# Performance work log

Measured on AMD Instinct MI355X. Metric: run time of the kernel, lower is better.

Reference implementation:

```python
import jax, jax.numpy as jnp
import numpy as np

# dims (match init_kwargs / input_specs)
B, T = 32, 512
DIM, DEPTH, HEADS, NB_FEAT, N_MASKS = 256, 6, 8, 128, 4
DIM_HEAD = DIM // HEADS  # 32
FF_MULT = 4
KERNEL_EPS = 1e-4


def _orth_proj(key, m, d):
    # FAVOR+ gaussian orthogonal random features: stacked QR blocks, row norms from fresh gaussians
    nb = m // d
    keys = jax.random.split(key, nb + 1)
    blocks = []
    for i in range(nb):
        g = jax.random.normal(keys[i], (d, d))
        q, _ = jnp.linalg.qr(g)
        blocks.append(q.T)
    proj = jnp.concatenate(blocks, axis=0)  # (m, d)
    norms = jnp.linalg.norm(jax.random.normal(keys[-1], (m, d)), axis=-1)
    return (proj * norms[:, None]).astype(jnp.float32)


def setup_inputs() -> dict:
    key = jax.random.key(0)
    ks = jax.random.split(key, 12)
    init = lambda k, sh: (jax.random.normal(k, sh, dtype=jnp.float32) * 0.02)
    L = DEPTH
    return {
        "mel": jax.random.normal(ks[0], (B, DIM, T), dtype=jnp.float32),
        "proj": _orth_proj(ks[1], NB_FEAT, DIM_HEAD),
        "ln1_g": jnp.ones((L, DIM), jnp.float32), "ln1_b": jnp.zeros((L, DIM), jnp.float32),
        "Wq": init(ks[2], (L, DIM, DIM)), "Wk": init(ks[3], (L, DIM, DIM)),
        "Wv": init(ks[4], (L, DIM, DIM)),
        "Wo": init(ks[5], (L, DIM, DIM)), "bo": jnp.zeros((L, DIM), jnp.float32),
        "ln2_g": jnp.ones((L, DIM), jnp.float32), "ln2_b": jnp.zeros((L, DIM), jnp.float32),
        "W1": init(ks[6], (L, DIM, FF_MULT * DIM)), "b1": jnp.zeros((L, FF_MULT * DIM), jnp.float32),
        "W2": init(ks[7], (L, FF_MULT * DIM, DIM)), "b2": jnp.zeros((L, DIM), jnp.float32),
        "Wm": init(ks[8], (DIM, N_MASKS)), "bm": jnp.zeros((N_MASKS,), jnp.float32),
    }


def _ln(x, g, b):
    mu = jnp.mean(x, -1, keepdims=True)
    var = jnp.var(x, -1, keepdims=True)
    return (x - mu) * jax.lax.rsqrt(var + 1e-5) * g + b


def _softmax_kernel(x, proj, is_query):
    # x: (B,H,N,dh), proj: (m,dh)
    dn = x.shape[-1] ** -0.25
    ratio = proj.shape[0] ** -0.5
    xd = jnp.einsum('bhnd,md->bhnm', x * dn, proj)
    diag = 0.5 * jnp.sum(jnp.square(x * dn), axis=-1, keepdims=True)
    if is_query:
        mx = jnp.max(xd, axis=-1, keepdims=True)
    else:
        mx = jnp.max(xd, axis=(-1, -2), keepdims=True)
    return ratio * (jnp.exp(xd - diag - mx) + KERNEL_EPS)


def _split_heads(x):
    b, n, _ = x.shape
    return x.reshape(b, n, HEADS, DIM_HEAD).transpose(0, 2, 1, 3)  # (B,H,N,dh)


def _forward(mel, proj, ln1_g, ln1_b, Wq, Wk, Wv, Wo, bo, ln2_g, ln2_b, W1, b1, W2, b2, Wm, bm):
    x = jnp.transpose(mel, (0, 2, 1))  # (B, T, DIM)
    for l in range(DEPTH):
        # --- FAVOR+ self-attention (pre-LN, non-causal linear attention) ---
        h = _ln(x, ln1_g[l], ln1_b[l])
        q = _split_heads(h @ Wq[l])
        k = _split_heads(h @ Wk[l])
        v = _split_heads(h @ Wv[l])
        qp = _softmax_kernel(q, proj, True)   # (B,H,T,m)
        kp = _softmax_kernel(k, proj, False)  # (B,H,T,m)
        ctx = jnp.einsum('bhnm,bhnd->bhmd', kp, v)          # (B,H,m,dh)
        o = jnp.einsum('bhnm,bhmd->bhnd', qp, ctx)          # (B,H,T,dh)
        denom = jnp.einsum('bhnm,bhm->bhn', qp, kp.sum(axis=2))
        o = o / denom[..., None]
        o = o.transpose(0, 2, 1, 3).reshape(x.shape[0], x.shape[1], DIM)
        x = x + o @ Wo[l] + bo[l]
        h = _ln(x, ln2_g[l], ln2_b[l])
        x = x + jax.nn.gelu(h @ W1[l] + b1[l]) @ W2[l] + b2[l]
    masks = x @ Wm + bm                  # (B, T, M)
    return jnp.transpose(masks, (0, 2, 1))  # (B, M, T)


def reference(mel, proj, ln1_g, ln1_b, Wq, Wk, Wv, Wo, bo, ln2_g, ln2_b, W1, b1, W2, b2, Wm, bm):
    return _forward(mel, proj, ln1_g, ln1_b, Wq, Wk, Wv, Wo, bo, ln2_g, ln2_b, W1, b1, W2, b2, Wm, bm)
```

## Files before the change

kernel.cpp:

```cpp
#include <hip/hip_runtime.h>
#include <math.h>

#define B 32
#define T 512
#define D 256
#define H 8
#define DH 32
#define MF 128
#define NLAYER 6
#define FF 1024
#define NM 4
#define BT (B*T)
#define BH (B*H)

#define DN2H 0.08838834764831845f
#define DNS  0.4204482076268573f
#define RATIO 0.08838834764831845f
#define KEPS 1e-4f

typedef __attribute__((ext_vector_type(8))) short short8;
typedef __attribute__((ext_vector_type(4))) float f32x4;

#define MFMA(a, b, c) __builtin_amdgcn_mfma_f32_16x16x32_bf16(a, b, c, 0, 0, 0)

#define SWZG(l) (((((l) & 3) + (((l) >> 3) & 3)) & 3) * 8)
#define RS(li, gi) (((((gi) - ((li) >> 1)) & 3)) * 8)

#define WAIT_VM(N) asm volatile("s_waitcnt vmcnt(" #N ")" ::: "memory")

__device__ __forceinline__ ushort f2b(float x) {
  union { float f; unsigned u; } c; c.f = x;
  unsigned r = (c.u + 0x7FFFu + ((c.u >> 16) & 1u)) >> 16;
  return (ushort)r;
}
__device__ __forceinline__ float bf2f(ushort u) {
  union { unsigned u; float f; } c; c.u = ((unsigned)u) << 16;
  return c.f;
}
__device__ __forceinline__ void gload16(const ushort* g, ushort* l) {
  __builtin_amdgcn_global_load_lds((const __attribute__((address_space(1))) void*)g,
                                   (__attribute__((address_space(3))) void*)l, 16, 0, 0);
}

__global__ void transpose_mel(const float* __restrict__ mel, float* __restrict__ x) {
  __shared__ float tile[32][33];
  int b = blockIdx.z;
  int d0 = blockIdx.y * 32, t0 = blockIdx.x * 32;
  int tx = threadIdx.x, ty = threadIdx.y;
  #pragma unroll
  for (int i = 0; i < 32; i += 8)
    tile[ty + i][tx] = mel[(b * D + d0 + ty + i) * T + t0 + tx];
  __syncthreads();
  #pragma unroll
  for (int i = 0; i < 32; i += 8)
    x[(b * T + t0 + ty + i) * D + d0 + tx] = tile[tx][ty + i];
}

__global__ void wtrans(const float* __restrict__ W, ushort* __restrict__ WT,
                       int K, int N, size_t lin, size_t lout) {
  __shared__ float tile[32][33];
  int l = blockIdx.z;
  const float* Wl = W + (size_t)l * lin;
  ushort* WTl = WT + (size_t)l * lout;
  int k0 = blockIdx.y * 32, n0 = blockIdx.x * 32;
  int tx = threadIdx.x, ty = threadIdx.y;
  #pragma unroll
  for (int i = 0; i < 32; i += 8)
    tile[ty + i][tx] = Wl[(size_t)(k0 + ty + i) * N + n0 + tx];
  __syncthreads();
  #pragma unroll
  for (int i = 0; i < 32; i += 8)
    WTl[(size_t)(n0 + ty + i) * K + k0 + tx] = f2b(tile[tx][ty + i]);
}

__global__ void proj_conv(const float* __restrict__ proj, ushort* __restrict__ projd) {
  int e = blockIdx.x * 256 + threadIdx.x;
  if (e < MF * DH) projd[e] = f2b(proj[e] * DNS);
}

__global__ __launch_bounds__(256) void ln_kernel(const float* __restrict__ x, const float* __restrict__ g,
                          const float* __restrict__ bb, ushort* __restrict__ y) {
  int row = blockIdx.x * 4 + (threadIdx.x >> 6);
  int lane = threadIdx.x & 63;
  const float4 v = ((const float4*)(x + (size_t)row * D))[lane];
  float s = v.x + v.y + v.z + v.w;
  #pragma unroll
  for (int off = 32; off; off >>= 1) s += __shfl_down(s, off);
  s = __shfl(s, 0);
  float mu = s * (1.0f / 256.0f);
  float dx = v.x - mu, dy = v.y - mu, dz = v.z - mu, dw = v.w - mu;
  float q = dx * dx + dy * dy + dz * dz + dw * dw;
  #pragma unroll
  for (int off = 32; off; off >>= 1) q += __shfl_down(q, off);
  q = __shfl(q, 0);
  float rstd = rsqrtf(q * (1.0f / 256.0f) + 1e-5f);
  const float4 gg = ((const float4*)g)[lane];
  const float4 be = ((const float4*)bb)[lane];
  ushort4 o;
  o.x = f2b(dx * rstd * gg.x + be.x);
  o.y = f2b(dy * rstd * gg.y + be.y);
  o.z = f2b(dz * rstd * gg.z + be.z);
  o.w = f2b(dw * rstd * gg.w + be.w);
  ((ushort4*)(y + (size_t)row * D))[lane] = o;
}

template<int EPI, int BM>
__global__ __launch_bounds__(256) void gemm_bf16(
    const ushort* __restrict__ A, const ushort* __restrict__ BTm,
    const float* __restrict__ bias,
    ushort* __restrict__ outB,
    ushort* __restrict__ qo, ushort* __restrict__ ko, ushort* __restrict__ vT,
    int N, int K) {
  constexpr int MFR = BM / 32;
  __shared__ __align__(16) ushort Al[2][BM * 32];
  __shared__ __align__(16) ushort Bl[2][128 * 32];
  int tid = threadIdx.x;
  int wave = tid >> 6, lane = tid & 63;
  int wr = wave >> 1, wc = wave & 1;
  int gi = lane >> 4, li = lane & 15;
  int lrow = lane >> 2, lkb = SWZG(lane);
  int row0 = blockIdx.y * BM, col0 = blockIdx.x * 128;
  f32x4 acc[MFR][4] = {};

  auto stage = [&](int buf, int kk) {
    #pragma unroll
    for (int i = 0; i < BM / 64; i++) {
      int chunk = wave * (BM / 64) + i;
      gload16(&A[(size_t)(row0 + chunk * 16 + lrow) * K + kk + lkb], &Al[buf][chunk * 512]);
    }
    #pragma unroll
    for (int i = 0; i < 2; i++) {
      int chunk = wave * 2 + i;
      gload16(&BTm[(size_t)(col0 + chunk * 16 + lrow) * K + kk + lkb], &Bl[buf][chunk * 512]);
    }
  };

  stage(0, 0);
  int cur = 0;
  for (int k0 = 0; k0 < K; k0 += 32, cur ^= 1) {
    if (k0 + 32 < K) {
      stage(cur ^ 1, k0 + 32);
      if (BM == 64) { WAIT_VM(3); } else { WAIT_VM(4); }
    } else {
      WAIT_VM(0);
    }
    __builtin_amdgcn_s_barrier();
    __builtin_amdgcn_sched_barrier(0);
    short8 a[MFR], b[4];
    #pragma unroll
    for (int m = 0; m < MFR; m++)
      a[m] = *(const short8*)&Al[cur][(wr * (MFR * 16) + m * 16 + li) * 32 + RS(li, gi)];
    #pragma unroll
    for (int n = 0; n < 4; n++)
      b[n] = *(const short8*)&Bl[cur][(wc * 64 + n * 16 + li) * 32 + RS(li, gi)];
    #pragma unroll
    for (int m = 0; m < MFR; m++)
      #pragma unroll
      for (int n = 0; n < 4; n++)
        acc[m][n] = MFMA(a[m], b[n], acc[m][n]);
    __builtin_amdgcn_s_barrier();
  }
  #pragma unroll
  for (int m = 0; m < MFR; m++) {
    int rbase = row0 + wr * (MFR * 16) + m * 16 + gi * 4;
    #pragma unroll
    for (int n = 0; n < 4; n++) {
      int col = col0 + wc * 64 + n * 16 + li;
      f32x4 v = acc[m][n];
      if (EPI == 2) {
        float bs = bias[col];
        #pragma unroll
        for (int r = 0; r < 4; r++) {
          float u = v[r] + bs;
          float p = u + 0.044715f * u * u * u;
          float gel = u / (1.0f + __expf(-1.5957691216057308f * p));
          outB[(size_t)(rbase + r) * N + col] = f2b(gel);
        }
      } else {
        if (col < 256) {
          #pragma unroll
          for (int r = 0; r < 4; r++) qo[(size_t)(rbase + r) * 256 + col] = f2b(v[r]);
        } else if (col < 512) {
          #pragma unroll
          for (int r = 0; r < 4; r++) ko[(size_t)(rbase + r) * 256 + col - 256] = f2b(v[r]);
        } else {
          int b_ = rbase >> 9, t = rbase & 511;
          int hh = (col - 512) >> 5, d = (col - 512) & 31;
          ushort4 pk;
          pk.x = f2b(v[0]); pk.y = f2b(v[1]); pk.z = f2b(v[2]); pk.w = f2b(v[3]);
          *(ushort4*)&vT[((size_t)((b_ * 8 + hh) * 32 + d)) * 512 + t] = pk;
        }
      }
    }
  }
}

__global__ __launch_bounds__(256) void ctx_fused(
    const ushort* __restrict__ kb, const ushort* __restrict__ projd,
    const ushort* __restrict__ vT, ushort* __restrict__ Bmat) {
  __shared__ __align__(16) ushort Kl[512 * 32];
  __shared__ __align__(16) ushort Pl[128 * 32];
  __shared__ __align__(16) ushort Sl[2][128 * 40];
  __shared__ __align__(16) ushort Bvl[2][32 * 32];
  __shared__ float dg_s[512];
  __shared__ float red_s[256];
  int bh = blockIdx.x;
  int b = bh >> 3, h = bh & 7;
  int tid = threadIdx.x, wave = tid >> 6, lane = tid & 63;
  int gi = lane >> 4, li = lane & 15;
  int lrow = lane >> 2, lkb = (lane & 3) * 8;
  const ushort* Kg = kb + (size_t)(b * 512) * 256 + h * 32;
  const ushort* Vg = vT + (size_t)bh * 32 * 512;
  #pragma unroll
  for (int i = 0; i < 8; i++) {
    int chunk = wave * 8 + i;
    gload16(&Kg[(size_t)(chunk * 16 + lrow) * 256 + lkb], &Kl[chunk * 512]);
  }
  #pragma unroll
  for (int i = 0; i < 2; i++) {
    int chunk = wave * 2 + i;
    gload16(&projd[(chunk * 16 + lrow) * 32 + lkb], &Pl[chunk * 512]);
  }
  __syncthreads();
  #pragma unroll
  for (int i = 0; i < 2; i++) {
    int t = tid * 2 + i;
    const ushort* kr = &Kl[t * 32];
    float s = 0.f;
    #pragma unroll
    for (int j = 0; j < 32; j++) { float v = bf2f(kr[j]); s += v * v; }
    dg_s[t] = DN2H * s;
  }
  short8 bp0 = *(const short8*)&Pl[(wave * 32 + li) * 32 + gi * 8];
  short8 bp1 = *(const short8*)&Pl[(wave * 32 + 16 + li) * 32 + gi * 8];
  float smax = -1e30f;
  for (int c = 0; c < 16; c++) {
    int t0c = c * 32;
    short8 a0 = *(const short8*)&Kl[(t0c + li) * 32 + gi * 8];
    short8 a1 = *(const short8*)&Kl[(t0c + 16 + li) * 32 + gi * 8];
    f32x4 s00 = {}, s01 = {}, s10 = {}, s11 = {};
    s00 = MFMA(a0, bp0, s00); s01 = MFMA(a0, bp1, s01);
    s10 = MFMA(a1, bp0, s10); s11 = MFMA(a1, bp1, s11);
    #pragma unroll
    for (int r = 0; r < 4; r++)
      smax = fmaxf(smax, fmaxf(fmaxf(s00[r], s01[r]), fmaxf(s10[r], s11[r])));
  }
  red_s[tid] = smax;
  __syncthreads();
  for (int s = 128; s; s >>= 1) {
    if (tid < s) red_s[tid] = fmaxf(red_s[tid], red_s[tid + s]);
    __syncthreads();
  }
  float km = red_s[0];
  f32x4 cacc[2][2] = {};
  float ks0 = 0.f, ks1 = 0.f;
  int cur = 0;
  for (int c = 0; c < 16; c++, cur ^= 1) {
    int t0c = c * 32;
    if (wave < 2)
      gload16(&Vg[(size_t)(wave * 16 + lrow) * 512 + t0c + lkb], &Bvl[cur][wave * 512]);
    short8 a0 = *(const short8*)&Kl[(t0c + li) * 32 + gi * 8];
    short8 a1 = *(const short8*)&Kl[(t0c + 16 + li) * 32 + gi * 8];
    f32x4 s00 = {}, s01 = {}, s10 = {}, s11 = {};
    s00 = MFMA(a0, bp0, s00); s01 = MFMA(a0, bp1, s01);
    s10 = MFMA(a1, bp0, s10); s11 = MFMA(a1, bp1, s11);
    ushort4 w00, w01, w10, w11;
    #pragma unroll
    for (int r = 0; r < 4; r++) {
      float d0 = dg_s[t0c + gi * 4 + r];
      float d1 = dg_s[t0c + 16 + gi * 4 + r];
      float k00 = RATIO * (__expf(s00[r] - d0 - km) + KEPS);
      float k01 = RATIO * (__expf(s01[r] - d0 - km) + KEPS);
      float k10 = RATIO * (__expf(s10[r] - d1 - km) + KEPS);
      float k11 = RATIO * (__expf(s11[r] - d1 - km) + KEPS);
      ks0 += k00 + k10; ks1 += k01 + k11;
      ((ushort*)&w00)[r] = f2b(k00); ((ushort*)&w01)[r] = f2b(k01);
      ((ushort*)&w10)[r] = f2b(k10); ((ushort*)&w11)[r] = f2b(k11);
    }
    *(ushort4*)&Sl[cur][(wave * 32 + li) * 40 + gi * 4]           = w00;
    *(ushort4*)&Sl[cur][(wave * 32 + 16 + li) * 40 + gi * 4]      = w01;
    *(ushort4*)&Sl[cur][(wave * 32 + li) * 40 + 16 + gi * 4]      = w10;
    *(ushort4*)&Sl[cur][(wave * 32 + 16 + li) * 40 + 16 + gi * 4] = w11;
    __syncthreads();
    short8 ca0 = *(const short8*)&Sl[cur][(wave * 32 + li) * 40 + gi * 8];
    short8 ca1 = *(const short8*)&Sl[cur][(wave * 32 + 16 + li) * 40 + gi * 8];
    short8 cb0 = *(const short8*)&Bvl[cur][li * 32 + gi * 8];
    short8 cb1 = *(const short8*)&Bvl[cur][(16 + li) * 32 + gi * 8];
    cacc[0][0] = MFMA(ca0, cb0, cacc[0][0]);
    cacc[0][1] = MFMA(ca0, cb1, cacc[0][1]);
    cacc[1][0] = MFMA(ca1, cb0, cacc[1][0]);
    cacc[1][1] = MFMA(ca1, cb1, cacc[1][1]);
  }
  ks0 += __shfl_xor(ks0, 16); ks0 += __shfl_xor(ks0, 32);
  ks1 += __shfl_xor(ks1, 16); ks1 += __shfl_xor(ks1, 32);
  if (gi == 0) {
    Bmat[((size_t)bh * 48 + 32) * 128 + wave * 32 + li] = f2b(ks0);
    Bmat[((size_t)bh * 48 + 32) * 128 + wave * 32 + 16 + li] = f2b(ks1);
  }
  #pragma unroll
  for (int m = 0; m < 2; m++)
    #pragma unroll
    for (int n = 0; n < 2; n++) {
      int dd = n * 16 + li;
      int mg = wave * 32 + m * 16 + gi * 4;
      ushort4 pk;
      pk.x = f2b(cacc[m][n][0]); pk.y = f2b(cacc[m][n][1]);
      pk.z = f2b(cacc[m][n][2]); pk.w = f2b(cacc[m][n][3]);
      *(ushort4*)&Bmat[((size_t)bh * 48 + dd) * 128 + mg] = pk;
    }
  for (int e = tid; e < 15 * 128; e += 256)
    Bmat[((size_t)bh * 48 + 33) * 128 + e] = 0;
}

__global__ __launch_bounds__(256) void favq_o(
    const ushort* __restrict__ qb, const ushort* __restrict__ projd,
    const ushort* __restrict__ Bmat, ushort* __restrict__ ob) {
  __shared__ __align__(16) ushort Ql[64 * 32];
  __shared__ __align__(16) ushort Pl[128 * 32];
  __shared__ __align__(16) ushort Sl[64 * 136];
  __shared__ __align__(16) ushort Bml[48 * 136];
  __shared__ float dgq[64];
  int bh = blockIdx.y;
  int t0 = blockIdx.x * 64;
  int b = bh >> 3, h = bh & 7;
  int tid = threadIdx.x, wave = tid >> 6, lane = tid & 63;
  int gi = lane >> 4, li = lane & 15;
  int lrow = lane >> 2, lkb = (lane & 3) * 8;
  const ushort* Qg = qb + (size_t)(b * 512) * 256 + h * 32;
  gload16(&Qg[(size_t)(t0 + wave * 16 + lrow) * 256 + lkb], &Ql[wave * 512]);
  #pragma unroll
  for (int i = 0; i < 2; i++) {
    int chunk = wave * 2 + i;
    gload16(&projd[(chunk * 16 + lrow) * 32 + lkb], &Pl[chunk * 512]);
  }
  #pragma unroll
  for (int j = 0; j < 3; j++) {
    int c = j * 256 + tid;
    int r = c >> 4, g = c & 15;
    *(uint4*)&Bml[r * 136 + g * 8] = *(const uint4*)&Bmat[(size_t)bh * 48 * 128 + r * 128 + g * 8];
  }
  __syncthreads();
  if (tid < 64) {
    const ushort* qr = &Ql[tid * 32];
    float s = 0.f;
    #pragma unroll
    for (int j = 0; j < 32; j++) { float v = bf2f(qr[j]); s += v * v; }
    dgq[tid] = DN2H * s;
  }
  short8 bq = *(const short8*)&Ql[(wave * 16 + li) * 32 + gi * 8];
  f32x4 sacc[8] = {};
  #pragma unroll
  for (int m = 0; m < 8; m++) {
    short8 a = *(const short8*)&Pl[(m * 16 + li) * 32 + gi * 8];
    sacc[m] = MFMA(a, bq, sacc[m]);
  }
  __syncthreads();
  float mx = -1e30f;
  #pragma unroll
  for (int m = 0; m < 8; m++)
    #pragma unroll
    for (int r = 0; r < 4; r++) mx = fmaxf(mx, sacc[m][r]);
  mx = fmaxf(mx, __shfl_xor(mx, 16));
  mx = fmaxf(mx, __shfl_xor(mx, 32));
  float dg = dgq[wave * 16 + li];
  #pragma unroll
  for (int m = 0; m < 8; m++) {
    ushort4 o4;
    #pragma unroll
    for (int r = 0; r < 4; r++)
      ((ushort*)&o4)[r] = f2b(RATIO * (__expf(sacc[m][r] - dg - mx) + KEPS));
    *(ushort4*)&Sl[(wave * 16 + li) * 136 + m * 16 + gi * 4] = o4;
  }
  __syncthreads();
  f32x4 oacc[3] = {};
  #pragma unroll
  for (int ks = 0; ks < 4; ks++) {
    short8 a = *(const short8*)&Sl[(wave * 16 + li) * 136 + ks * 32 + gi * 8];
    #pragma unroll
    for (int n = 0; n < 3; n++) {
      short8 bb = *(const short8*)&Bml[(n * 16 + li) * 136 + ks * 32 + gi * 8];
      oacc[n] = MFMA(a, bb, oacc[n]);
    }
  }
  int t = t0 + wave * 16 + gi * 4;
  float den[4];
  #pragma unroll
  for (int r = 0; r < 4; r++) den[r] = __shfl(oacc[2][r], lane & 48);
  #pragma unroll
  for (int n = 0; n < 2; n++)
    #pragma unroll
    for (int r = 0; r < 4; r++)
      ob[((size_t)(b * 512) + t + r) * 256 + h * 32 + n * 16 + li] = f2b(oacc[n][r] / den[r]);
}

__global__ __launch_bounds__(256) void wo_ff1(
    const ushort* __restrict__ ob, const ushort* __restrict__ woT,
    const float* __restrict__ bo, const float* __restrict__ res, float* __restrict__ x,
    const float* __restrict__ g, const float* __restrict__ bvec,
    const ushort* __restrict__ w1T, const float* __restrict__ b1v,
    ushort* __restrict__ ffh) {
  __shared__ __align__(16) ushort Apr[4][2][1024];
  __shared__ __align__(16) ushort Bpr[4][2][2048];
  __shared__ __align__(16) ushort Hp[8 * 1024];
  __shared__ float rs1[4 * 32], rs2[4 * 32];
  int tid = threadIdx.x, wave = tid >> 6, lane = tid & 63;
  int gi = lane >> 4, li = lane & 15;
  int lrow = lane >> 2, lkb = SWZG(lane);
  int row0 = blockIdx.x * 32;
  f32x4 acc[2][4] = {};

  auto stage1 = [&](int buf, int kk) {
    #pragma unroll
    for (int i = 0; i < 2; i++)
      gload16(&ob[(size_t)(row0 + i * 16 + lrow) * 256 + kk + lkb], &Apr[wave][buf][i * 512]);
    #pragma unroll
    for (int i = 0; i < 4; i++)
      gload16(&woT[(size_t)(wave * 64 + i * 16 + lrow) * 256 + kk + lkb], &Bpr[wave][buf][i * 512]);
  };
  stage1(0, 0);
  int cur = 0;
  for (int k0 = 0; k0 < 256; k0 += 32, cur ^= 1) {
    if (k0 + 32 < 256) { stage1(cur ^ 1, k0 + 32); WAIT_VM(6); }
    else { WAIT_VM(0); }
    __builtin_amdgcn_sched_barrier(0);
    short8 a[2], b[4];
    #pragma unroll
    for (int m = 0; m < 2; m++)
      a[m] = *(const short8*)&Apr[wave][cur][(m * 16 + li) * 32 + RS(li, gi)];
    #pragma unroll
    for (int n = 0; n < 4; n++)
      b[n] = *(const short8*)&Bpr[wave][cur][(n * 16 + li) * 32 + RS(li, gi)];
    #pragma unroll
    for (int m = 0; m < 2; m++)
      #pragma unroll
      for (int n = 0; n < 4; n++)
        acc[m][n] = MFMA(a[m], b[n], acc[m][n]);
  }
  #pragma unroll
  for (int m = 0; m < 2; m++) {
    #pragma unroll
    for (int r = 0; r < 4; r++) {
      int row = row0 + m * 16 + gi * 4 + r;
      int ridx = m * 16 + gi * 4 + r;
      float s1 = 0.f, s2 = 0.f;
      #pragma unroll
      for (int n = 0; n < 4; n++) {
        int col = wave * 64 + n * 16 + li;
        float val = acc[m][n][r] + bo[col] + res[(size_t)row * 256 + col];
        acc[m][n][r] = val;
        s1 += val; s2 += val * val;
      }
      #pragma unroll
      for (int off = 1; off <= 8; off <<= 1) { s1 += __shfl_xor(s1, off); s2 += __shfl_xor(s2, off); }
      if (li == 0) { rs1[wave * 32 + ridx] = s1; rs2[wave * 32 + ridx] = s2; }
    }
  }
  __syncthreads();
  {
    float g4[4], bv4[4];
    #pragma unroll
    for (int n = 0; n < 4; n++) {
      int col = wave * 64 + n * 16 + li;
      g4[n] = g[col]; bv4[n] = bvec[col];
    }
    #pragma unroll
    for (int m = 0; m < 2; m++) {
      #pragma unroll
      for (int r = 0; r < 4; r++) {
        int row32 = m * 16 + gi * 4 + r;
        int row = row0 + row32;
        float t1 = rs1[row32] + rs1[32 + row32] + rs1[64 + row32] + rs1[96 + row32];
        float t2 = rs2[row32] + rs2[32 + row32] + rs2[64 + row32] + rs2[96 + row32];
        float mu = t1 * (1.f / 256.f);
        float rstd = rsqrtf(t2 * (1.f / 256.f) - mu * mu + 1e-5f);
        #pragma unroll
        for (int n = 0; n < 4; n++) {
          int col = wave * 64 + n * 16 + li;
          float val = acc[m][n][r];
          x[(size_t)row * 256 + col] = val;
          float hv = (val - mu) * rstd * g4[n] + bv4[n];
          int kc = col >> 5, c32 = col & 31;
          int G = c32 >> 3, c7 = c32 & 7;
          int slot = (G - (row32 >> 1)) & 3;
          Hp[kc * 1024 + row32 * 32 + slot * 8 + c7] = f2b(hv);
        }
      }
    }
  }
  auto stage2 = [&](int buf, int st) {
    int nc = st >> 3, ks = st & 7;
    #pragma unroll
    for (int i = 0; i < 4; i++)
      gload16(&w1T[(size_t)(nc * 256 + wave * 64 + i * 16 + lrow) * 256 + ks * 32 + lkb],
              &Bpr[wave][buf][i * 512]);
  };
  stage2(0, 0);
  __syncthreads();
  cur = 0;
  f32x4 fac[2][4] = {};
  for (int st = 0; st < 32; st++, cur ^= 1) {
    int nc = st >> 3, ks = st & 7;
    if (st + 1 < 32) { stage2(cur ^ 1, st + 1); WAIT_VM(4); }
    else { WAIT_VM(0); }
    __builtin_amdgcn_sched_barrier(0);
    short8 a[2], b[4];
    #pragma unroll
    for (int m = 0; m < 2; m++)
      a[m] = *(const short8*)&Hp[ks * 1024 + (m * 16 + li) * 32 + RS(li, gi)];
    #pragma unroll
    for (int n = 0; n < 4; n++)
      b[n] = *(const short8*)&Bpr[wave][cur][(n * 16 + li) * 32 + RS(li, gi)];
    #pragma unroll
    for (int m = 0; m < 2; m++)
      #pragma unroll
      for (int n = 0; n < 4; n++)
        fac[m][n] = MFMA(a[m], b[n], fac[m][n]);
    if (ks == 7) {
      #pragma unroll
      for (int m = 0; m < 2; m++) {
        int rbase = row0 + m * 16 + gi * 4;
        #pragma unroll
        for (int n = 0; n < 4; n++) {
          int col = nc * 256 + wave * 64 + n * 16 + li;
          float bs = b1v[col];
          #pragma unroll
          for (int r = 0; r < 4; r++) {
            float u = fac[m][n][r] + bs;
            float p = u + 0.044715f * u * u * u;
            float gel = u / (1.0f + __expf(-1.5957691216057308f * p));
            ffh[(size_t)(rbase + r) * 1024 + col] = f2b(gel);
            fac[m][n][r] = 0.f;
          }
        }
      }
    }
  }
}

__global__ __launch_bounds__(256) void ff2_qkv(
    const ushort* __restrict__ ffh, const ushort* __restrict__ w2T,
    const float* __restrict__ b2v, const float* __restrict__ res, float* __restrict__ x,
    const float* __restrict__ g, const float* __restrict__ bvec,
    const ushort* __restrict__ qkvT,
    ushort* __restrict__ qo, ushort* __restrict__ ko, ushort* __restrict__ vT) {
  __shared__ __align__(16) ushort Apr[4][2][1024];
  __shared__ __align__(16) ushort Bpr[4][2][2048];
  __shared__ __align__(16) ushort Hp[8 * 1024];
  __shared__ float rs1[4 * 32], rs2[4 * 32];
  int tid = threadIdx.x, wave = tid >> 6, lane = tid & 63;
  int gi = lane >> 4, li = lane & 15;
  int lrow = lane >> 2, lkb = SWZG(lane);
  int row0 = blockIdx.x * 32;
  f32x4 acc[2][4] = {};

  auto stage1 = [&](int buf, int kk) {
    #pragma unroll
    for (int i = 0; i < 2; i++)
      gload16(&ffh[(size_t)(row0 + i * 16 + lrow) * 1024 + kk + lkb], &Apr[wave][buf][i * 512]);
    #pragma unroll
    for (int i = 0; i < 4; i++)
      gload16(&w2T[(size_t)(wave * 64 + i * 16 + lrow) * 1024 + kk + lkb], &Bpr[wave][buf][i * 512]);
  };
  stage1(0, 0);
  int cur = 0;
  for (int k0 = 0; k0 < 1024; k0 += 32, cur ^= 1) {
    if (k0 + 32 < 1024) { stage1(cur ^ 1, k0 + 32); WAIT_VM(6); }
    else { WAIT_VM(0); }
    __builtin_amdgcn_sched_barrier(0);
    short8 a[2], b[4];
    #pragma unroll
    for (int m = 0; m < 2; m++)
      a[m] = *(const short8*)&Apr[wave][cur][(m * 16 + li) * 32 + RS(li, gi)];
    #pragma unroll
    for (int n = 0; n < 4; n++)
      b[n] = *(const short8*)&Bpr[wave][cur][(n * 16 + li) * 32 + RS(li, gi)];
    #pragma unroll
    for (int m = 0; m < 2; m++)
      #pragma unroll
      for (int n = 0; n < 4; n++)
        acc[m][n] = MFMA(a[m], b[n], acc[m][n]);
  }
  #pragma unroll
  for (int m = 0; m < 2; m++) {
    #pragma unroll
    for (int r = 0; r < 4; r++) {
      int row = row0 + m * 16 + gi * 4 + r;
      int ridx = m * 16 + gi * 4 + r;
      float s1 = 0.f, s2 = 0.f;
      #pragma unroll
      for (int n = 0; n < 4; n++) {
        int col = wave * 64 + n * 16 + li;
        float val = acc[m][n][r] + b2v[col] + res[(size_t)row * 256 + col];
        acc[m][n][r] = val;
        s1 += val; s2 += val * val;
      }
      #pragma unroll
      for (int off = 1; off <= 8; off <<= 1) { s1 += __shfl_xor(s1, off); s2 += __shfl_xor(s2, off); }
      if (li == 0) { rs1[wave * 32 + ridx] = s1; rs2[wave * 32 + ridx] = s2; }
    }
  }
  __syncthreads();
  {
    float g4[4], bv4[4];
    #pragma unroll
    for (int n = 0; n < 4; n++) {
      int col = wave * 64 + n * 16 + li;
      g4[n] = g[col]; bv4[n] = bvec[col];
    }
    #pragma unroll
    for (int m = 0; m < 2; m++) {
      #pragma unroll
      for (int r = 0; r < 4; r++) {
        int row32 = m * 16 + gi * 4 + r;
        int row = row0 + row32;
        float t1 = rs1[row32] + rs1[32 + row32] + rs1[64 + row32] + rs1[96 + row32];
        float t2 = rs2[row32] + rs2[32 + row32] + rs2[64 + row32] + rs2[96 + row32];
        float mu = t1 * (1.f / 256.f);
        float rstd = rsqrtf(t2 * (1.f / 256.f) - mu * mu + 1e-5f);
        #pragma unroll
        for (int n = 0; n < 4; n++) {
          int col = wave * 64 + n * 16 + li;
          float val = acc[m][n][r];
          x[(size_t)row * 256 + col] = val;
          float hv = (val - mu) * rstd * g4[n] + bv4[n];
          int kc = col >> 5, c32 = col & 31;
          int G = c32 >> 3, c7 = c32 & 7;
          int slot = (G - (row32 >> 1)) & 3;
          Hp[kc * 1024 + row32 * 32 + slot * 8 + c7] = f2b(hv);
        }
      }
    }
  }
  auto stage2 = [&](int buf, int st) {
    int nc = st >> 3, ks = st & 7;
    #pragma unroll
    for (int i = 0; i < 4; i++)
      gload16(&qkvT[(size_t)(nc * 256 + wave * 64 + i * 16 + lrow) * 256 + ks * 32 + lkb],
              &Bpr[wave][buf][i * 512]);
  };
  stage2(0, 0);
  __syncthreads();
  cur = 0;
  f32x4 fac[2][4] = {};
  for (int st = 0; st < 24; st++, cur ^= 1) {
    int nc = st >> 3, ks = st & 7;
    if (st + 1 < 24) { stage2(cur ^ 1, st + 1); WAIT_VM(4); }
    else { WAIT_VM(0); }
    __builtin_amdgcn_sched_barrier(0);
    short8 a[2], b[4];
    #pragma unroll
    for (int m = 0; m < 2; m++)
      a[m] = *(const short8*)&Hp[ks * 1024 + (m * 16 + li) * 32 + RS(li, gi)];
    #pragma unroll
    for (int n = 0; n < 4; n++)
      b[n] = *(const short8*)&Bpr[wave][cur][(n * 16 + li) * 32 + RS(li, gi)];
    #pragma unroll
    for (int m = 0; m < 2; m++)
      #pragma unroll
      for (int n = 0; n < 4; n++)
        fac[m][n] = MFMA(a[m], b[n], fac[m][n]);
    if (ks == 7) {
      #pragma unroll
      for (int m = 0; m < 2; m++) {
        int rbase = row0 + m * 16 + gi * 4;
        #pragma unroll
        for (int n = 0; n < 4; n++) {
          int col256 = wave * 64 + n * 16 + li;
          if (nc == 0) {
            #pragma unroll
            for (int r = 0; r < 4; r++) { qo[(size_t)(rbase + r) * 256 + col256] = f2b(fac[m][n][r]); fac[m][n][r] = 0.f; }
          } else if (nc == 1) {
            #pragma unroll
            for (int r = 0; r < 4; r++) { ko[(size_t)(rbase + r) * 256 + col256] = f2b(fac[m][n][r]); fac[m][n][r] = 0.f; }
          } else {
            int b_ = rbase >> 9, t = rbase & 511;
            int hh = col256 >> 5, d = col256 & 31;
            ushort4 pk;
            pk.x = f2b(fac[m][n][0]); pk.y = f2b(fac[m][n][1]);
            pk.z = f2b(fac[m][n][2]); pk.w = f2b(fac[m][n][3]);
            *(ushort4*)&vT[((size_t)((b_ * 8 + hh) * 32 + d)) * 512 + t] = pk;
            fac[m][n][0] = fac[m][n][1] = fac[m][n][2] = fac[m][n][3] = 0.f;
          }
        }
      }
    }
  }
}

__global__ __launch_bounds__(256) void gemm_mask(
    const ushort* __restrict__ A, const ushort* __restrict__ BTm,
    const float* __restrict__ bias, const float* __restrict__ res,
    const float* __restrict__ Wm, const float* __restrict__ bm, float* __restrict__ mout,
    int K) {
  __shared__ __align__(16) ushort Al[2][32 * 32];
  __shared__ __align__(16) ushort Bl[2][256 * 32];
  __shared__ float pmS[4 * 128];
  int tid = threadIdx.x, wave = tid >> 6, lane = tid & 63;
  int gi = lane >> 4, li = lane & 15;
  int lrow = lane >> 2, lkb = SWZG(lane);
  int row0 = blockIdx.x * 32;
  int wc = wave;
  f32x4 acc[2][4] = {};

  auto stage = [&](int buf, int kk) {
    if (wave < 2)
      gload16(&A[(size_t)(row0 + wave * 16 + lrow) * K + kk + lkb], &Al[buf][wave * 512]);
    #pragma unroll
    for (int i = 0; i < 4; i++) {
      int chunk = wave * 4 + i;
      gload16(&BTm[(size_t)(chunk * 16 + lrow) * K + kk + lkb], &Bl[buf][chunk * 512]);
    }
  };
  stage(0, 0);
  __syncthreads();
  int cur = 0;
  for (int k0 = 0; k0 < K; k0 += 32, cur ^= 1) {
    if (k0 + 32 < K) stage(cur ^ 1, k0 + 32);
    short8 a[2], b[4];
    #pragma unroll
    for (int m = 0; m < 2; m++)
      a[m] = *(const short8*)&Al[cur][(m * 16 + li) * 32 + RS(li, gi)];
    #pragma unroll
    for (int n = 0; n < 4; n++)
      b[n] = *(const short8*)&Bl[cur][(wc * 64 + n * 16 + li) * 32 + RS(li, gi)];
    #pragma unroll
    for (int m = 0; m < 2; m++)
      #pragma unroll
      for (int n = 0; n < 4; n++)
        acc[m][n] = MFMA(a[m], b[n], acc[m][n]);
    __syncthreads();
  }
  #pragma unroll
  for (int m = 0; m < 2; m++) {
    #pragma unroll
    for (int r = 0; r < 4; r++) {
      int row = row0 + m * 16 + gi * 4 + r;
      int ridx = m * 16 + gi * 4 + r;
      #pragma unroll
      for (int n = 0; n < 4; n++) {
        int col = wc * 64 + n * 16 + li;
        acc[m][n][r] += bias[col] + res[(size_t)row * 256 + col];
      }
      #pragma unroll
      for (int msk = 0; msk < NM; msk++) {
        float sm = 0.f;
        #pragma unroll
        for (int n = 0; n < 4; n++) {
          int col = wc * 64 + n * 16 + li;
          sm += acc[m][n][r] * Wm[col * NM + msk];
        }
        #pragma unroll
        for (int off = 1; off <= 8; off <<= 1) sm += __shfl_xor(sm, off);
        if (li == 0) pmS[wave * 128 + ridx * 4 + msk] = sm;
      }
    }
  }
  __syncthreads();
  if (tid < 128) {
    int ridx = tid >> 2, msk = tid & 3;
    float tot = pmS[ridx * 4 + msk] + pmS[128 + ridx * 4 + msk] +
                pmS[256 + ridx * 4 + msk] + pmS[384 + ridx * 4 + msk];
    int grow = row0 + ridx;
    int bb_ = grow >> 9, t = grow & 511;
    mout[((size_t)(bb_ * NM) + msk) * 512 + t] = tot + bm[msk];
  }
}

extern "C" void kernel_launch(void* const* d_in, const int* in_sizes, int n_in,
                              void* d_out, int out_size, void* d_ws, size_t ws_size,
                              hipStream_t stream) {
  const float* mel   = (const float*)d_in[0];
  const float* proj  = (const float*)d_in[1];
  const float* ln1_g = (const float*)d_in[2];
  const float* ln1_b = (const float*)d_in[3];
  const float* Wq    = (const float*)d_in[4];
  const float* Wk    = (const float*)d_in[5];
  const float* Wv    = (const float*)d_in[6];
  const float* Wo    = (const float*)d_in[7];
  const float* bo    = (const float*)d_in[8];
  const float* ln2_g = (const float*)d_in[9];
  const float* ln2_b = (const float*)d_in[10];
  const float* W1    = (const float*)d_in[11];
  const float* b1    = (const float*)d_in[12];
  const float* W2    = (const float*)d_in[13];
  const float* b2    = (const float*)d_in[14];
  const float* Wm    = (const float*)d_in[15];
  const float* bm    = (const float*)d_in[16];

  float* x      = (float*)d_ws;
  ushort* us    = (ushort*)(x + (size_t)BT * D);
  ushort* h     = us;                   us += (size_t)BT * D;
  ushort* qb    = us;                   us += (size_t)BT * D;
  ushort* kb    = us;                   us += (size_t)BT * D;
  ushort* vT    = us;                   us += (size_t)BH * 32 * T;
  ushort* ob    = us;                   us += (size_t)BT * D;
  ushort* ffh   = us;                   us += (size_t)BT * FF;
  ushort* Bmat  = us;                   us += (size_t)BH * 48 * MF;
  ushort* qkvT  = us;                   us += (size_t)NLAYER * 768 * 256;
  ushort* woT   = us;                   us += (size_t)NLAYER * 256 * 256;
  ushort* w1T   = us;                   us += (size_t)NLAYER * 1024 * 256;
  ushort* w2T   = us;                   us += (size_t)NLAYER * 256 * 1024;
  ushort* projd = us;                   us += (size_t)MF * DH;

  wtrans<<<dim3(8, 8, NLAYER), dim3(32, 8), 0, stream>>>(Wq, qkvT, 256, 256, 65536, 768 * 256);
  wtrans<<<dim3(8, 8, NLAYER), dim3(32, 8), 0, stream>>>(Wk, qkvT + 256 * 256, 256, 256, 65536, 768 * 256);
  wtrans<<<dim3(8, 8, NLAYER), dim3(32, 8), 0, stream>>>(Wv, qkvT + 512 * 256, 256, 256, 65536, 768 * 256);
  wtrans<<<dim3(8, 8, NLAYER), dim3(32, 8), 0, stream>>>(Wo, woT, 256, 256, 65536, 65536);
  wtrans<<<dim3(32, 8, NLAYER), dim3(32, 8), 0, stream>>>(W1, w1T, 256, 1024, 262144, 262144);
  wtrans<<<dim3(8, 32, NLAYER), dim3(32, 8), 0, stream>>>(W2, w2T, 1024, 256, 262144, 262144);
  proj_conv<<<16, 256, 0, stream>>>(proj, projd);

  transpose_mel<<<dim3(T / 32, D / 32, B), dim3(32, 8), 0, stream>>>(mel, x);
  ln_kernel<<<BT / 4, 256, 0, stream>>>(x, ln1_g, ln1_b, h);

  gemm_bf16<0, 64><<<dim3(6, 256), 256, 0, stream>>>(h, qkvT,
      nullptr, nullptr, qb, kb, vT, 768, 256);

  for (int l = 0; l < NLAYER; l++) {
    ctx_fused<<<BH, 256, 0, stream>>>(kb, projd, vT, Bmat);
    favq_o<<<dim3(8, BH), 256, 0, stream>>>(qb, projd, Bmat, ob);
    wo_ff1<<<BT / 32, 256, 0, stream>>>(ob, woT + (size_t)l * 256 * 256,
        bo + l * D, x, x, ln2_g + l * D, ln2_b + l * D,
        w1T + (size_t)l * 1024 * 256, b1 + (size_t)l * FF, ffh);
    if (l < NLAYER - 1) {
      ff2_qkv<<<BT / 32, 256, 0, stream>>>(ffh, w2T + (size_t)l * 256 * 1024,
          b2 + l * D, x, x, ln1_g + (l + 1) * D, ln1_b + (l + 1) * D,
          qkvT + (size_t)(l + 1) * 768 * 256, qb, kb, vT);
    } else {
      gemm_mask<<<BT / 32, 256, 0, stream>>>(ffh, w2T + (size_t)l * 256 * 1024,
          b2 + l * D, x, Wm, bm, (float*)d_out, 1024);
    }
  }
}
```

Measured before the change: 698.9 us.

## Load GEMM operands directly from global into registers instead of LDS staging

In the fused Wo+LN+FF1 and FF2+LN+QKV kernels, the per-wave LDS double buffers fed by async global-to-LDS copies are removed. MFMA operand fragments are now loaded straight from global memory into registers, with a two-deep register prefetch. This cuts LDS usage, which may raise occupancy, and drops the LDS round trip and wait-count handling. The cost is that each wave issues uncoalesced 16-byte row loads that depend on caches to absorb reuse, and more registers are held live.

```diff
diff --git a/kernel.cpp b/kernel.cpp
--- a/kernel.cpp
+++ b/kernel.cpp
@@ -399,42 +399,41 @@
     const float* __restrict__ g, const float* __restrict__ bvec,
     const ushort* __restrict__ w1T, const float* __restrict__ b1v,
     ushort* __restrict__ ffh) {
-  __shared__ __align__(16) ushort Apr[4][2][1024];
-  __shared__ __align__(16) ushort Bpr[4][2][2048];
   __shared__ __align__(16) ushort Hp[8 * 1024];
   __shared__ float rs1[4 * 32], rs2[4 * 32];
   int tid = threadIdx.x, wave = tid >> 6, lane = tid & 63;
   int gi = lane >> 4, li = lane & 15;
-  int lrow = lane >> 2, lkb = SWZG(lane);
   int row0 = blockIdx.x * 32;
   f32x4 acc[2][4] = {};
 
-  auto stage1 = [&](int buf, int kk) {
-    #pragma unroll
-    for (int i = 0; i < 2; i++)
-      gload16(&ob[(size_t)(row0 + i * 16 + lrow) * 256 + kk + lkb], &Apr[wave][buf][i * 512]);
-    #pragma unroll
-    for (int i = 0; i < 4; i++)
-      gload16(&woT[(size_t)(wave * 64 + i * 16 + lrow) * 256 + kk + lkb], &Bpr[wave][buf][i * 512]);
+  auto ldA1 = [&](short8* a, int st) {
+    #pragma unroll
+    for (int m = 0; m < 2; m++)
+      a[m] = *(const short8*)&ob[(size_t)(row0 + m * 16 + li) * 256 + st * 32 + gi * 8];
   };
-  stage1(0, 0);
-  int cur = 0;
-  for (int k0 = 0; k0 < 256; k0 += 32, cur ^= 1) {
-    if (k0 + 32 < 256) { stage1(cur ^ 1, k0 + 32); WAIT_VM(6); }
-    else { WAIT_VM(0); }
-    __builtin_amdgcn_sched_barrier(0);
-    short8 a[2], b[4];
-    #pragma unroll
-    for (int m = 0; m < 2; m++)
-      a[m] = *(const short8*)&Apr[wave][cur][(m * 16 + li) * 32 + RS(li, gi)];
+  auto ldB1 = [&](short8* b, int st) {
     #pragma unroll
     for (int n = 0; n < 4; n++)
-      b[n] = *(const short8*)&Bpr[wave][cur][(n * 16 + li) * 32 + RS(li, gi)];
-    #pragma unroll
-    for (int m = 0; m < 2; m++)
-      #pragma unroll
-      for (int n = 0; n < 4; n++)
-        acc[m][n] = MFMA(a[m], b[n], acc[m][n]);
+      b[n] = *(const short8*)&woT[(size_t)(wave * 64 + n * 16 + li) * 256 + st * 32 + gi * 8];
+  };
+  {
+    short8 A0[2], B0[4], A1[2], B1[4];
+    ldA1(A0, 0); ldB1(B0, 0);
+    #pragma unroll
+    for (int st = 0; st < 8; st += 2) {
+      ldA1(A1, st + 1); ldB1(B1, st + 1);
+      #pragma unroll
+      for (int m = 0; m < 2; m++)
+        #pragma unroll
+        for (int n = 0; n < 4; n++)
+          acc[m][n] = MFMA(A0[m], B0[n], acc[m][n]);
+      if (st + 2 < 8) { ldA1(A0, st + 2); ldB1(B0, st + 2); }
+      #pragma unroll
+      for (int m = 0; m < 2; m++)
+        #pragma unroll
+        for (int n = 0; n < 4; n++)
+          acc[m][n] = MFMA(A1[m], B1[n], acc[m][n]);
+    }
   }
   #pragma unroll
   for (int m = 0; m < 2; m++) {
@@ -487,49 +486,59 @@
       }
     }
   }
-  auto stage2 = [&](int buf, int st) {
+  auto ldB2 = [&](short8* b, int st) {
     int nc = st >> 3, ks = st & 7;
     #pragma unroll
-    for (int i = 0; i < 4; i++)
-      gload16(&w1T[(size_t)(nc * 256 + wave * 64 + i * 16 + lrow) * 256 + ks * 32 + lkb],
-              &Bpr[wave][buf][i * 512]);
+    for (int n = 0; n < 4; n++)
+      b[n] = *(const short8*)&w1T[(size_t)(nc * 256 + wave * 64 + n * 16 + li) * 256 + ks * 32 + gi * 8];
   };
-  stage2(0, 0);
-  __syncthreads();
-  cur = 0;
-  f32x4 fac[2][4] = {};
-  for (int st = 0; st < 32; st++, cur ^= 1) {
-    int nc = st >> 3, ks = st & 7;
-    if (st + 1 < 32) { stage2(cur ^ 1, st + 1); WAIT_VM(4); }
-    else { WAIT_VM(0); }
-    __builtin_amdgcn_sched_barrier(0);
-    short8 a[2], b[4];
-    #pragma unroll
-    for (int m = 0; m < 2; m++)
-      a[m] = *(const short8*)&Hp[ks * 1024 + (m * 16 + li) * 32 + RS(li, gi)];
-    #pragma unroll
-    for (int n = 0; n < 4; n++)
-      b[n] = *(const short8*)&Bpr[wave][cur][(n * 16 + li) * 32 + RS(li, gi)];
-    #pragma unroll
-    for (int m = 0; m < 2; m++)
-      #pragma unroll
-      for (int n = 0; n < 4; n++)
-        fac[m][n] = MFMA(a[m], b[n], fac[m][n]);
-    if (ks == 7) {
-      #pragma unroll
-      for (int m = 0; m < 2; m++) {
-        int rbase = row0 + m * 16 + gi * 4;
-        #pragma unroll
-        for (int n = 0; n < 4; n++) {
-          int col = nc * 256 + wave * 64 + n * 16 + li;
-          float bs = b1v[col];
+  {
+    short8 B0[4], B1[4];
+    ldB2(B0, 0);
+    __syncthreads();
+    f32x4 fac[2][4] = {};
+    for (int st = 0; st < 32; st += 2) {
+      int ks0s = st & 7, ks1s = (st + 1) & 7, nc1 = (st + 1) >> 3;
+      ldB2(B1, st + 1);
+      {
+        short8 a[2];
+        #pragma unroll
+        for (int m = 0; m < 2; m++)
+          a[m] = *(const short8*)&Hp[ks0s * 1024 + (m * 16 + li) * 32 + RS(li, gi)];
+        #pragma unroll
+        for (int m = 0; m < 2; m++)
           #pragma unroll
-          for (int r = 0; r < 4; r++) {
-            float u = fac[m][n][r] + bs;
-            float p = u + 0.044715f * u * u * u;
-            float gel = u / (1.0f + __expf(-1.5957691216057308f * p));
-            ffh[(size_t)(rbase + r) * 1024 + col] = f2b(gel);
-            fac[m][n][r] = 0.f;
+          for (int n = 0; n < 4; n++)
+            fac[m][n] = MFMA(a[m], B0[n], fac[m][n]);
+      }
+      if (st + 2 < 32) ldB2(B0, st + 2);
+      {
+        short8 a[2];
+        #pragma unroll
+        for (int m = 0; m < 2; m++)
+          a[m] = *(const short8*)&Hp[ks1s * 1024 + (m * 16 + li) * 32 + RS(li, gi)];
+        #pragma unroll
+        for (int m = 0; m < 2; m++)
+          #pragma unroll
+          for (int n = 0; n < 4; n++)
+            fac[m][n] = MFMA(a[m], B1[n], fac[m][n]);
+      }
+      if (ks1s == 7) {
+        #pragma unroll
+        for (int m = 0; m < 2; m++) {
+          int rbase = row0 + m * 16 + gi * 4;
+          #pragma unroll
+          for (int n = 0; n < 4; n++) {
+            int col = nc1 * 256 + wave * 64 + n * 16 + li;
+            float bs = b1v[col];
+            #pragma unroll
+            for (int r = 0; r < 4; r++) {
+              float u = fac[m][n][r] + bs;
+              float p = u + 0.044715f * u * u * u;
+              float gel = u / (1.0f + __expf(-1.5957691216057308f * p));
+              ffh[(size_t)(rbase + r) * 1024 + col] = f2b(gel);
+              fac[m][n][r] = 0.f;
+            }
           }
         }
       }
@@ -543,42 +552,40 @@
     const float* __restrict__ g, const float* __restrict__ bvec,
     const ushort* __restrict__ qkvT,
     ushort* __restrict__ qo, ushort* __restrict__ ko, ushort* __restrict__ vT) {
-  __shared__ __align__(16) ushort Apr[4][2][1024];
-  __shared__ __align__(16) ushort Bpr[4][2][2048];
   __shared__ __align__(16) ushort Hp[8 * 1024];
   __shared__ float rs1[4 * 32], rs2[4 * 32];
   int tid = threadIdx.x, wave = tid >> 6, lane = tid & 63;
   int gi = lane >> 4, li = lane & 15;
-  int lrow = lane >> 2, lkb = SWZG(lane);
   int row0 = blockIdx.x * 32;
   f32x4 acc[2][4] = {};
 
-  auto stage1 = [&](int buf, int kk) {
-    #pragma unroll
-    for (int i = 0; i < 2; i++)
-      gload16(&ffh[(size_t)(row0 + i * 16 + lrow) * 1024 + kk + lkb], &Apr[wave][buf][i * 512]);
-    #pragma unroll
-    for (int i = 0; i < 4; i++)
-      gload16(&w2T[(size_t)(wave * 64 + i * 16 + lrow) * 1024 + kk + lkb], &Bpr[wave][buf][i * 512]);
+  auto ldA1 = [&](short8* a, int st) {
+    #pragma unroll
+    for (int m = 0; m < 2; m++)
+      a[m] = *(const short8*)&ffh[(size_t)(row0 + m * 16 + li) * 1024 + st * 32 + gi * 8];
   };
-  stage1(0, 0);
-  int cur = 0;
-  for (int k0 = 0; k0 < 1024; k0 += 32, cur ^= 1) {
-    if (k0 + 32 < 1024) { stage1(cur ^ 1, k0 + 32); WAIT_VM(6); }
-    else { WAIT_VM(0); }
-    __builtin_amdgcn_sched_barrier(0);
-    short8 a[2], b[4];
-    #pragma unroll
-    for (int m = 0; m < 2; m++)
-      a[m] = *(const short8*)&Apr[wave][cur][(m * 16 + li) * 32 + RS(li, gi)];
+  auto ldB1 = [&](short8* b, int st) {
     #pragma unroll
     for (int n = 0; n < 4; n++)
-      b[n] = *(const short8*)&Bpr[wave][cur][(n * 16 + li) * 32 + RS(li, gi)];
-    #pragma unroll
-    for (int m = 0; m < 2; m++)
-      #pragma unroll
-      for (int n = 0; n < 4; n++)
-        acc[m][n] = MFMA(a[m], b[n], acc[m][n]);
+      b[n] = *(const short8*)&w2T[(size_t)(wave * 64 + n * 16 + li) * 1024 + st * 32 + gi * 8];
+  };
+  {
+    short8 A0[2], B0[4], A1[2], B1[4];
+    ldA1(A0, 0); ldB1(B0, 0);
+    for (int st = 0; st < 32; st += 2) {
+      ldA1(A1, st + 1); ldB1(B1, st + 1);
+      #pragma unroll
+      for (int m = 0; m < 2; m++)
+        #pragma unroll
+        for (int n = 0; n < 4; n++)
+          acc[m][n] = MFMA(A0[m], B0[n], acc[m][n]);
+      if (st + 2 < 32) { ldA1(A0, st + 2); ldB1(B0, st + 2); }
+      #pragma unroll
+      for (int m = 0; m < 2; m++)
+        #pragma unroll
+        for (int n = 0; n < 4; n++)
+          acc[m][n] = MFMA(A1[m], B1[n], acc[m][n]);
+    }
   }
   #pragma unroll
   for (int m = 0; m < 2; m++) {
@@ -631,55 +638,65 @@
       }
     }
   }
-  auto stage2 = [&](int buf, int st) {
+  auto ldB2 = [&](short8* b, int st) {
     int nc = st >> 3, ks = st & 7;
     #pragma unroll
-    for (int i = 0; i < 4; i++)
-      gload16(&qkvT[(size_t)(nc * 256 + wave * 64 + i * 16 + lrow) * 256 + ks * 32 + lkb],
-              &Bpr[wave][buf][i * 512]);
+    for (int n = 0; n < 4; n++)
+      b[n] = *(const short8*)&qkvT[(size_t)(nc * 256 + wave * 64 + n * 16 + li) * 256 + ks * 32 + gi * 8];
   };
-  stage2(0, 0);
-  __syncthreads();
-  cur = 0;
-  f32x4 fac[2][4] = {};
-  for (int st = 0; st < 24; st++, cur ^= 1) {
-    int nc = st >> 3, ks = st & 7;
-    if (st + 1 < 24) { stage2(cur ^ 1, st + 1); WAIT_VM(4); }
-    else { WAIT_VM(0); }
-    __builtin_amdgcn_sched_barrier(0);
-    short8 a[2], b[4];
-    #pragma unroll
-    for (int m = 0; m < 2; m++)
-      a[m] = *(const short8*)&Hp[ks * 1024 + (m * 16 + li) * 32 + RS(li, gi)];
-    #pragma unroll
-    for (int n = 0; n < 4; n++)
-      b[n] = *(const short8*)&Bpr[wave][cur][(n * 16 + li) * 32 + RS(li, gi)];
-    #pragma unroll
-    for (int m = 0; m < 2; m++)
-      #pragma unroll
-      for (int n = 0; n < 4; n++)
-        fac[m][n] = MFMA(a[m], b[n], fac[m][n]);
-    if (ks == 7) {
-      #pragma unroll
-      for (int m = 0; m < 2; m++) {
-        int rbase = row0 + m * 16 + gi * 4;
-        #pragma unroll
-        for (int n = 0; n < 4; n++) {
-          int col256 = wave * 64 + n * 16 + li;
-          if (nc == 0) {
-            #pragma unroll
-            for (int r = 0; r < 4; r++) { qo[(size_t)(rbase + r) * 256 + col256] = f2b(fac[m][n][r]); fac[m][n][r] = 0.f; }
-          } else if (nc == 1) {
-            #pragma unroll
-            for (int r = 0; r < 4; r++) { ko[(size_t)(rbase + r) * 256 + col256] = f2b(fac[m][n][r]); fac[m][n][r] = 0.f; }
-          } else {
-            int b_ = rbase >> 9, t = rbase & 511;
-            int hh = col256 >> 5, d = col256 & 31;
-            ushort4 pk;
-            pk.x = f2b(fac[m][n][0]); pk.y = f2b(fac[m][n][1]);
-            pk.z = f2b(fac[m][n][2]); pk.w = f2b(fac[m][n][3]);
-            *(ushort4*)&vT[((size_t)((b_ * 8 + hh) * 32 + d)) * 512 + t] = pk;
-            fac[m][n][0] = fac[m][n][1] = fac[m][n][2] = fac[m][n][3] = 0.f;
+  {
+    short8 B0[4], B1[4];
+    ldB2(B0, 0);
+    __syncthreads();
+    f32x4 fac[2][4] = {};
+    for (int st = 0; st < 24; st += 2) {
+      int ks0s = st & 7, ks1s = (st + 1) & 7, nc1 = (st + 1) >> 3;
+      ldB2(B1, st + 1);
+      {
+        short8 a[2];
+        #pragma unroll
+        for (int m = 0; m < 2; m++)
+          a[m] = *(const short8*)&Hp[ks0s * 1024 + (m * 16 + li) * 32 + RS(li, gi)];
+        #pragma unroll
+        for (int m = 0; m < 2; m++)
+          #pragma unroll
+          for (int n = 0; n < 4; n++)
+            fac[m][n] = MFMA(a[m], B0[n], fac[m][n]);
+      }
+      if (st + 2 < 24) ldB2(B0, st + 2);
+      {
+        short8 a[2];
+        #pragma unroll
+        for (int m = 0; m < 2; m++)
+          a[m] = *(const short8*)&Hp[ks1s * 1024 + (m * 16 + li) * 32 + RS(li, gi)];
+        #pragma unroll
+        for (int m = 0; m < 2; m++)
+          #pragma unroll
+          for (int n = 0; n < 4; n++)
+            fac[m][n] = MFMA(a[m], B1[n], fac[m][n]);
+      }
+      if (ks1s == 7) {
+        #pragma unroll
+        for (int m = 0; m < 2; m++) {
+          int rbase = row0 + m * 16 + gi * 4;
+          #pragma unroll
+          for (int n = 0; n < 4; n++) {
+            int col256 = wave * 64 + n * 16 + li;
+            if (nc1 == 0) {
+              #pragma unroll
+              for (int r = 0; r < 4; r++) { qo[(size_t)(rbase + r) * 256 + col256] = f2b(fac[m][n][r]); fac[m][n][r] = 0.f; }
+            } else if (nc1 == 1) {
+              #pragma unroll
+              for (int r = 0; r < 4; r++) { ko[(size_t)(rbase + r) * 256 + col256] = f2b(fac[m][n][r]); fac[m][n][r] = 0.f; }
+            } else {
+              int b_ = rbase >> 9, t = rbase & 511;
+              int hh = col256 >> 5, d = col256 & 31;
+              ushort4 pk;
+              pk.x = f2b(fac[m][n][0]); pk.y = f2b(fac[m][n][1]);
+              pk.z = f2b(fac[m][n][2]); pk.w = f2b(fac[m][n][3]);
+              *(ushort4*)&vT[((size_t)((b_ * 8 + hh) * 32 + d)) * 512 + t] = pk;
+              fac[m][n][0] = fac[m][n][1] = fac[m][n][2] = fac[m][n][3] = 0.f;
+            }
           }
         }
       }
```

Result: slower. 942.1 us (+34.8%).

## Replace two-pass key max with online running-max rescaling in ctx_fused

Applied to the files above, without the earlier changes.

The separate pass that recomputed the K·proj MFMAs just to find the global key max is removed, along with its shared-memory tree reduction. In its place, each chunk computes a block-wide max and rescales the context and key-sum accumulators whenever the running max grows. The KEPS term is moved out of the loop: column sums of V are accumulated with an all-ones MFMA and the epsilon and ratio are applied once at the end. In exchange, each of the 16 loop iterations gains an extra block barrier plus a wave shuffle reduction, and bf16 rounding of the exponentials now happens relative to a changing max.

```diff
diff --git a/kernel.cpp b/kernel.cpp
--- a/kernel.cpp
+++ b/kernel.cpp
@@ -203,7 +203,7 @@
   __shared__ __align__(16) ushort Sl[2][128 * 40];
   __shared__ __align__(16) ushort Bvl[2][32 * 32];
   __shared__ float dg_s[512];
-  __shared__ float red_s[256];
+  __shared__ float wmax_s[4];
   int bh = blockIdx.x;
   int b = bh >> 3, h = bh & 7;
   int tid = threadIdx.x, wave = tid >> 6, lane = tid & 63;
@@ -233,26 +233,13 @@
   }
   short8 bp0 = *(const short8*)&Pl[(wave * 32 + li) * 32 + gi * 8];
   short8 bp1 = *(const short8*)&Pl[(wave * 32 + 16 + li) * 32 + gi * 8];
-  float smax = -1e30f;
-  for (int c = 0; c < 16; c++) {
-    int t0c = c * 32;
-    short8 a0 = *(const short8*)&Kl[(t0c + li) * 32 + gi * 8];
-    short8 a1 = *(const short8*)&Kl[(t0c + 16 + li) * 32 + gi * 8];
-    f32x4 s00 = {}, s01 = {}, s10 = {}, s11 = {};
-    s00 = MFMA(a0, bp0, s00); s01 = MFMA(a0, bp1, s01);
-    s10 = MFMA(a1, bp0, s10); s11 = MFMA(a1, bp1, s11);
-    #pragma unroll
-    for (int r = 0; r < 4; r++)
-      smax = fmaxf(smax, fmaxf(fmaxf(s00[r], s01[r]), fmaxf(s10[r], s11[r])));
-  }
-  red_s[tid] = smax;
-  __syncthreads();
-  for (int s = 128; s; s >>= 1) {
-    if (tid < s) red_s[tid] = fmaxf(red_s[tid], red_s[tid + s]);
-    __syncthreads();
-  }
-  float km = red_s[0];
+  short8 onesf;
+  #pragma unroll
+  for (int i = 0; i < 8; i++) onesf[i] = (short)0x3F80;
+
+  float m_run = -1e30f;
   f32x4 cacc[2][2] = {};
+  f32x4 cones[2] = {};
   float ks0 = 0.f, ks1 = 0.f;
   int cur = 0;
   for (int c = 0; c < 16; c++, cur ^= 1) {
@@ -264,18 +251,38 @@
     f32x4 s00 = {}, s01 = {}, s10 = {}, s11 = {};
     s00 = MFMA(a0, bp0, s00); s01 = MFMA(a0, bp1, s01);
     s10 = MFMA(a1, bp0, s10); s11 = MFMA(a1, bp1, s11);
+    float mv = -1e30f;
+    #pragma unroll
+    for (int r = 0; r < 4; r++)
+      mv = fmaxf(mv, fmaxf(fmaxf(s00[r], s01[r]), fmaxf(s10[r], s11[r])));
+    #pragma unroll
+    for (int msk = 1; msk <= 32; msk <<= 1) mv = fmaxf(mv, __shfl_xor(mv, msk));
+    if (lane == 0) wmax_s[wave] = mv;
+    __syncthreads();
+    float cmax = fmaxf(fmaxf(wmax_s[0], wmax_s[1]), fmaxf(wmax_s[2], wmax_s[3]));
+    if (cmax > m_run) {
+      float sc = __expf(m_run - cmax);
+      #pragma unroll
+      for (int m = 0; m < 2; m++)
+        #pragma unroll
+        for (int n = 0; n < 2; n++)
+          #pragma unroll
+          for (int r = 0; r < 4; r++) cacc[m][n][r] *= sc;
+      ks0 *= sc; ks1 *= sc;
+      m_run = cmax;
+    }
     ushort4 w00, w01, w10, w11;
     #pragma unroll
     for (int r = 0; r < 4; r++) {
       float d0 = dg_s[t0c + gi * 4 + r];
       float d1 = dg_s[t0c + 16 + gi * 4 + r];
-      float k00 = RATIO * (__expf(s00[r] - d0 - km) + KEPS);
-      float k01 = RATIO * (__expf(s01[r] - d0 - km) + KEPS);
-      float k10 = RATIO * (__expf(s10[r] - d1 - km) + KEPS);
-      float k11 = RATIO * (__expf(s11[r] - d1 - km) + KEPS);
-      ks0 += k00 + k10; ks1 += k01 + k11;
-      ((ushort*)&w00)[r] = f2b(k00); ((ushort*)&w01)[r] = f2b(k01);
-      ((ushort*)&w10)[r] = f2b(k10); ((ushort*)&w11)[r] = f2b(k11);
+      float e00 = __expf(s00[r] - d0 - m_run);
+      float e01 = __expf(s01[r] - d0 - m_run);
+      float e10 = __expf(s10[r] - d1 - m_run);
+      float e11 = __expf(s11[r] - d1 - m_run);
+      ks0 += e00 + e10; ks1 += e01 + e11;
+      ((ushort*)&w00)[r] = f2b(e00); ((ushort*)&w01)[r] = f2b(e01);
+      ((ushort*)&w10)[r] = f2b(e10); ((ushort*)&w11)[r] = f2b(e11);
     }
     *(ushort4*)&Sl[cur][(wave * 32 + li) * 40 + gi * 4]           = w00;
     *(ushort4*)&Sl[cur][(wave * 32 + 16 + li) * 40 + gi * 4]      = w01;
@@ -290,12 +297,14 @@
     cacc[0][1] = MFMA(ca0, cb1, cacc[0][1]);
     cacc[1][0] = MFMA(ca1, cb0, cacc[1][0]);
     cacc[1][1] = MFMA(ca1, cb1, cacc[1][1]);
+    cones[0] = MFMA(onesf, cb0, cones[0]);
+    cones[1] = MFMA(onesf, cb1, cones[1]);
   }
   ks0 += __shfl_xor(ks0, 16); ks0 += __shfl_xor(ks0, 32);
   ks1 += __shfl_xor(ks1, 16); ks1 += __shfl_xor(ks1, 32);
   if (gi == 0) {
-    Bmat[((size_t)bh * 48 + 32) * 128 + wave * 32 + li] = f2b(ks0);
-    Bmat[((size_t)bh * 48 + 32) * 128 + wave * 32 + 16 + li] = f2b(ks1);
+    Bmat[((size_t)bh * 48 + 32) * 128 + wave * 32 + li] = f2b(RATIO * (ks0 + KEPS * 512.f));
+    Bmat[((size_t)bh * 48 + 32) * 128 + wave * 32 + 16 + li] = f2b(RATIO * (ks1 + KEPS * 512.f));
   }
   #pragma unroll
   for (int m = 0; m < 2; m++)
@@ -304,8 +313,10 @@
       int dd = n * 16 + li;
       int mg = wave * 32 + m * 16 + gi * 4;
       ushort4 pk;
-      pk.x = f2b(cacc[m][n][0]); pk.y = f2b(cacc[m][n][1]);
-      pk.z = f2b(cacc[m][n][2]); pk.w = f2b(cacc[m][n][3]);
+      pk.x = f2b(RATIO * (cacc[m][n][0] + KEPS * cones[n][0]));
+      pk.y = f2b(RATIO * (cacc[m][n][1] + KEPS * cones[n][1]));
+      pk.z = f2b(RATIO * (cacc[m][n][2] + KEPS * cones[n][2]));
+      pk.w = f2b(RATIO * (cacc[m][n][3] + KEPS * cones[n][3]));
       *(ushort4*)&Bmat[((size_t)bh * 48 + dd) * 128 + mg] = pk;
     }
   for (int e = tid; e < 15 * 128; e += 256)
```

New measurement: 728.9 us. 4.3% more time.
